# Kernel optimization log

Measured on AMD Instinct MI355X. Metric: run time of the kernel, lower is better.

## Reference

```python
import jax, jax.numpy as jnp
import numpy as np

N = 50000      # nodes
E = 800000     # edges
F_IN = 128     # input features
H = 8          # heads
F = 16         # features per head
NEG_SLOPE = 0.2


def setup_inputs() -> dict:
    key = jax.random.key(0)
    k_x, k_ei, k_w, k_as, k_ad = jax.random.split(key, 5)
    x = jax.random.normal(k_x, (N, F_IN), dtype=jnp.float32)
    edge_index = jax.random.randint(k_ei, (2, E), 0, N, dtype=jnp.int64)
    # learned params (PyG GATConv: lin weight [H*F, F_in] no bias; att_src/att_dst [H, F]; out bias [H*F])
    glorot = lambda k, shp: jax.random.uniform(k, shp, jnp.float32, -1.0, 1.0) * np.sqrt(6.0 / (shp[-1] + shp[-2]))
    W = glorot(k_w, (H * F, F_IN))
    att_src = glorot(k_as, (H, F))
    att_dst = glorot(k_ad, (H, F))
    bias = jnp.zeros((H * F,), dtype=jnp.float32)  # bias_init = zeros_
    return {"x": x, "W": W, "att_src": att_src, "att_dst": att_dst, "bias": bias, "edge_index": edge_index}


def reference(x, W, att_src, att_dst, bias, edge_index):
    # linear projection, split heads: [N, H, F]
    h = (x @ W.T).reshape(N, H, F)
    # per-node attention logits: [N, H]
    a_src = jnp.einsum('nhf,hf->nh', h, att_src)
    a_dst = jnp.einsum('nhf,hf->nh', h, att_dst)
    src, dst = edge_index[0], edge_index[1]
    # edge scores + LeakyReLU: [E, H]
    e = a_src[src] + a_dst[dst]
    e = jnp.where(e >= 0, e, NEG_SLOPE * e)
    # segment softmax over incoming edges of each dst node
    m = jax.ops.segment_max(e, dst, num_segments=N)          # [N, H]
    ex = jnp.exp(e - m[dst])                                  # [E, H]
    denom = jax.ops.segment_sum(ex, dst, num_segments=N)     # [N, H]
    alpha = ex / (denom[dst] + 1e-16)                         # [E, H]
    # weighted scatter-aggregate of source features
    msg = alpha[:, :, None] * h[src]                          # [E, H, F]
    out = jax.ops.segment_sum(msg, dst, num_segments=N)      # [N, H, F]
    return out.reshape(N, H * F) + bias
```

## Files before the change

### kernel.cpp

```cpp
#include <hip/hip_runtime.h>

#define NEG_SLOPE 0.2f
#define HEADS 8
#define FEAT 16
#define HF 128
#define FIN 128
#define BROWS 64
#define PITCH 136
#define BSHIFT 6
#define BNODES 64
#define MAXBUCK 1024
#define EPT 16
#define SCAP 32
#define CAP 2048

typedef __bf16 bf16x8 __attribute__((ext_vector_type(8)));
typedef float  f32x4  __attribute__((ext_vector_type(4)));

__device__ __forceinline__ bool detect_i64(const int* ei) {
    return (ei[1] | ei[3] | ei[5] | ei[7]) == 0;
}
__device__ __forceinline__ int load_idx(const int* ei, long long pos, bool is64) {
    return is64 ? ei[2 * pos] : ei[pos];
}

__device__ __forceinline__ float bf2f(unsigned u) { return __uint_as_float(u << 16); }

__device__ __forceinline__ unsigned short f2bf(float f) {
    unsigned u = __float_as_uint(f);
    unsigned r = u + 0x7fffu + ((u >> 16) & 1u);
    return (unsigned short)(r >> 16);
}

__global__ __launch_bounds__(256) void proj_binsort_kernel(
    const float* __restrict__ x, const float* __restrict__ W,
    const float* __restrict__ att_src, const float* __restrict__ att_dst,
    unsigned short* __restrict__ hb, float* __restrict__ a_src,
    float* __restrict__ a_dst,
    const int* __restrict__ ei, unsigned* __restrict__ ebuf,
    int* __restrict__ cnt2, int N, int E, int nb, int nsb, int PB)
{
    __shared__ __align__(16) char smem[(BROWS + FIN) * PITCH * 2];
    const int t = threadIdx.x;

    if (blockIdx.x >= PB) {
        int* lh = (int*)smem;
        const int blk = blockIdx.x - PB;
        const bool is64 = detect_i64(ei);
        const int e0 = blk * (EPT * 256);

        for (int b = t; b < nb; b += 256) lh[b] = 0;
        __syncthreads();

#pragma unroll
        for (int i = 0; i < EPT; ++i) {
            const int e = e0 + i * 256 + t;
            if (e < E) {
                const unsigned s = (unsigned)load_idx(ei, e, is64);
                const unsigned d = (unsigned)load_idx(ei, (long long)E + e, is64);
                const unsigned pk = s | (d << 16);
                const int bkt = d >> BSHIFT;
                const int ofs = atomicAdd(&lh[bkt], 1);
                if (ofs < SCAP)
                    ebuf[((size_t)bkt * nsb + blk) * SCAP + ofs] = pk;
            }
        }
        __syncthreads();
        for (int b = t; b < nb; b += 256)
            cnt2[blk * MAXBUCK + b] = min(lh[b], SCAP);
        return;
    }

    unsigned short* xs  = (unsigned short*)smem;
    unsigned short* wsl = xs + BROWS * PITCH;
    const int n0 = blockIdx.x * BROWS;

#pragma unroll
    for (int i = 0; i < 8; ++i) {
        const int f4 = i * 256 + t;
        const int r = f4 >> 5, c4 = f4 & 31;
        const int rr = (n0 + r < N) ? (n0 + r) : (N - 1);
        const float4 v = ((const float4*)(x + (size_t)rr * FIN))[c4];
        unsigned short* p = &xs[r * PITCH + c4 * 4];
        p[0] = f2bf(v.x); p[1] = f2bf(v.y); p[2] = f2bf(v.z); p[3] = f2bf(v.w);
    }
#pragma unroll
    for (int i = 0; i < 16; ++i) {
        const int f4 = i * 256 + t;
        const int r = f4 >> 5, c4 = f4 & 31;
        const float4 v = ((const float4*)(W + (size_t)r * FIN))[c4];
        unsigned short* p = &wsl[r * PITCH + c4 * 4];
        p[0] = f2bf(v.x); p[1] = f2bf(v.y); p[2] = f2bf(v.z); p[3] = f2bf(v.w);
    }
    __syncthreads();

    const int w = t >> 6, lane = t & 63;
    const int lrow = lane & 15;
    const int lk = lane >> 4;
    const int r0 = w * 16;

    f32x4 acc[8];
#pragma unroll
    for (int i = 0; i < 8; ++i) { f32x4 z = {0.f, 0.f, 0.f, 0.f}; acc[i] = z; }

#pragma unroll
    for (int ks = 0; ks < 4; ++ks) {
        const int kb = ks * 32 + lk * 8;
        const bf16x8 af = *(const bf16x8*)&xs[(r0 + lrow) * PITCH + kb];
#pragma unroll
        for (int tt = 0; tt < 8; ++tt) {
            const bf16x8 bf = *(const bf16x8*)&wsl[(tt * 16 + lrow) * PITCH + kb];
            acc[tt] = __builtin_amdgcn_mfma_f32_16x16x32_bf16(af, bf, acc[tt], 0, 0, 0);
        }
    }
    __syncthreads();

#pragma unroll
    for (int tt = 0; tt < 8; ++tt) {
#pragma unroll
        for (int rg = 0; rg < 4; ++rg) {
            const int row = r0 + lk * 4 + rg;
            const int col = tt * 16 + lrow;
            xs[row * PITCH + col] = f2bf(acc[tt][rg]);
        }
    }
    __syncthreads();

#pragma unroll
    for (int i = 0; i < 8; ++i) {
        const int u4 = i * 256 + t;
        const int r = u4 >> 5, c4 = u4 & 31;
        if (n0 + r < N) {
            const unsigned short* p = &xs[r * PITCH + c4 * 4];
            ushort4 v; v.x = p[0]; v.y = p[1]; v.z = p[2]; v.w = p[3];
            ((ushort4*)hb)[(size_t)(n0 + r) * (HF / 4) + c4] = v;
        }
    }
#pragma unroll
    for (int i = 0; i < 2; ++i) {
        const int p = i * 256 + t;
        const int r = p >> 3, hd = p & 7;
        if (n0 + r < N) {
            float s = 0.f, d = 0.f;
#pragma unroll
            for (int j = 0; j < FEAT; ++j) {
                const float hv = bf2f(xs[r * PITCH + hd * FEAT + j]);
                s = fmaf(hv, att_src[hd * FEAT + j], s);
                d = fmaf(hv, att_dst[hd * FEAT + j], d);
            }
            a_src[(size_t)(n0 + r) * HEADS + hd] = s;
            a_dst[(size_t)(n0 + r) * HEADS + hd] = d;
        }
    }
}

__global__ __launch_bounds__(256) void bucket_agg(
    const unsigned* __restrict__ ebuf, const int* __restrict__ cnt2,
    const float* __restrict__ a_src, const float* __restrict__ a_dst,
    const unsigned short* __restrict__ hb, const float* __restrict__ bias,
    float* __restrict__ out, int N, int nsb)
{
    __shared__ int soff[256];
    __shared__ unsigned ubuf[CAP];
    __shared__ unsigned srt[CAP];
    __shared__ int cnts[BNODES], sc[BNODES], cur[BNODES];
    const int b = blockIdx.x;
    const int t = threadIdx.x;

    const int v = (t < nsb) ? cnt2[t * MAXBUCK + b] : 0;
    soff[t] = v;
    __syncthreads();
#pragma unroll
    for (int off = 1; off < 256; off <<= 1) {
        const int y = (t >= off) ? soff[t - off] : 0;
        __syncthreads();
        soff[t] += y;
        __syncthreads();
    }
    const int cntb = min(soff[255], CAP);
    const int myoff = soff[t] - v;
    __syncthreads();

    if (t < nsb && v > 0) {
        const unsigned* sp = ebuf + ((size_t)b * nsb + t) * SCAP;
        for (int j = 0; j < v; ++j) {
            const int o = myoff + j;
            if (o < CAP) ubuf[o] = sp[j];
        }
    }
    if (t < BNODES) cnts[t] = 0;
    __syncthreads();

    for (int j = t; j < cntb; j += 256)
        atomicAdd(&cnts[(ubuf[j] >> 16) & (BNODES - 1)], 1);
    __syncthreads();
    if (t < BNODES) sc[t] = cnts[t];
    __syncthreads();
#pragma unroll
    for (int off = 1; off < BNODES; off <<= 1) {
        const int y = (t < BNODES && t >= off) ? sc[t - off] : 0;
        __syncthreads();
        if (t < BNODES) sc[t] += y;
        __syncthreads();
    }
    if (t < BNODES) cur[t] = sc[t] - cnts[t];
    __syncthreads();
    for (int j = t; j < cntb; j += 256) {
        const unsigned p = ubuf[j];
        const int dl = (p >> 16) & (BNODES - 1);
        const int ofs = atomicAdd(&cur[dl], 1);
        srt[ofs] = p & 0xffffu;
    }
    __syncthreads();

    const int w = t >> 6, lane = t & 63;
    const int hd = lane >> 3;
    const float2 b2 = ((const float2*)bias)[lane];

#pragma unroll 1
    for (int i = 0; i < BNODES / 4; ++i) {
        const int dl = w * (BNODES / 4) + i;
        const int d = b * BNODES + dl;
        if (d >= N) break;
        const int end = sc[dl];
        const int beg = end - cnts[dl];
        const float adh = a_dst[d * HEADS + hd];

        float acc0 = 0.f, acc1 = 0.f, den = 0.f;
        int j = beg;
        for (; j + 8 <= end; j += 8) {
            int s[8]; unsigned p[8]; float wg[8];
#pragma unroll
            for (int k = 0; k < 8; ++k) s[k] = (int)srt[j + k];
#pragma unroll
            for (int k = 0; k < 8; ++k)
                p[k] = *(const unsigned*)(hb + (size_t)s[k] * HF + 2 * lane);
#pragma unroll
            for (int k = 0; k < 8; ++k) {
                float vv = a_src[s[k] * HEADS + hd] + adh;
                vv = vv >= 0.f ? vv : NEG_SLOPE * vv;
                wg[k] = __expf(vv);
            }
#pragma unroll
            for (int k = 0; k < 8; ++k) {
                acc0 = fmaf(wg[k], bf2f(p[k] & 0xffffu), acc0);
                acc1 = fmaf(wg[k], bf2f(p[k] >> 16),     acc1);
                den += wg[k];
            }
        }
        for (; j + 4 <= end; j += 4) {
            int s[4]; unsigned p[4]; float wg[4];
#pragma unroll
            for (int k = 0; k < 4; ++k) s[k] = (int)srt[j + k];
#pragma unroll
            for (int k = 0; k < 4; ++k)
                p[k] = *(const unsigned*)(hb + (size_t)s[k] * HF + 2 * lane);
#pragma unroll
            for (int k = 0; k < 4; ++k) {
                float vv = a_src[s[k] * HEADS + hd] + adh;
                vv = vv >= 0.f ? vv : NEG_SLOPE * vv;
                wg[k] = __expf(vv);
            }
#pragma unroll
            for (int k = 0; k < 4; ++k) {
                acc0 = fmaf(wg[k], bf2f(p[k] & 0xffffu), acc0);
                acc1 = fmaf(wg[k], bf2f(p[k] >> 16),     acc1);
                den += wg[k];
            }
        }
        for (; j < end; ++j) {
            const int s = (int)srt[j];
            const unsigned p = *(const unsigned*)(hb + (size_t)s * HF + 2 * lane);
            float vv = a_src[s * HEADS + hd] + adh;
            vv = vv >= 0.f ? vv : NEG_SLOPE * vv;
            const float wg = __expf(vv);
            acc0 = fmaf(wg, bf2f(p & 0xffffu), acc0);
            acc1 = fmaf(wg, bf2f(p >> 16), acc1);
            den += wg;
        }
        const float inv = 1.f / (den + 1e-16f);
        float2 o2;
        o2.x = fmaf(acc0, inv, b2.x);
        o2.y = fmaf(acc1, inv, b2.y);
        ((float2*)out)[(size_t)d * (HF / 2) + lane] = o2;
    }
}

extern "C" void kernel_launch(void* const* d_in, const int* in_sizes, int n_in,
                              void* d_out, int out_size, void* d_ws, size_t ws_size,
                              hipStream_t stream)
{
    const float* x       = (const float*)d_in[0];
    const float* W       = (const float*)d_in[1];
    const float* att_src = (const float*)d_in[2];
    const float* att_dst = (const float*)d_in[3];
    const float* bias    = (const float*)d_in[4];
    const int*   ei      = (const int*)d_in[5];
    float* out = (float*)d_out;

    const int N = in_sizes[0] / FIN;
    const int E = in_sizes[5] / 2;
    const int NBUCK = (N + BNODES - 1) >> BSHIFT;
    const int NSB = (E + EPT * 256 - 1) / (EPT * 256);
    const int PB = (N + BROWS - 1) / BROWS;

    char* ws = (char*)d_ws;
    unsigned short* hb = (unsigned short*)ws; ws += (size_t)N * HF * 2;
    unsigned* ebuf = (unsigned*)ws; ws += (size_t)NBUCK * NSB * SCAP * 4;
    int* cnt2      = (int*)ws;  ws += (size_t)NSB * MAXBUCK * sizeof(int);
    float* a_src  = (float*)ws; ws += (size_t)N * HEADS * sizeof(float);
    float* a_dst  = (float*)ws; ws += (size_t)N * HEADS * sizeof(float);

    hipLaunchKernelGGL(proj_binsort_kernel, dim3(PB + NSB), dim3(256), 0, stream,
                       x, W, att_src, att_dst, hb, a_src, a_dst,
                       ei, ebuf, cnt2, N, E, NBUCK, NSB, PB);
    hipLaunchKernelGGL(bucket_agg, dim3(NBUCK), dim3(256), 0, stream,
                       ebuf, cnt2, a_src, a_dst, hb, bias, out, N, NSB);
}
```

Measured before the change: 161.5 us.

## Halve destination buckets and replace shared-memory scans with wavefront shuffle scans

Bucket size drops from 64 to 32 destination nodes, which doubles the number of aggregation blocks and shrinks the per-bucket staging buffers and shared memory. The two block-level prefix scans, one over per-source-block counts and one over per-node counts, now use wavefront shuffle scans instead of shared-memory scans with a barrier at every step, removing many __syncthreads. The risks are smaller per-segment capacity (SCAP 20, CAP 1024), which could overflow on skewed degree distributions, and each block now does the same setup work for half as many nodes.

```diff
diff --git a/kernel.cpp b/kernel.cpp
--- a/kernel.cpp
+++ b/kernel.cpp
@@ -7,12 +7,12 @@
 #define FIN 128
 #define BROWS 64
 #define PITCH 136
-#define BSHIFT 6
-#define BNODES 64
-#define MAXBUCK 1024
+#define BSHIFT 5
+#define BNODES 32
+#define MAXBUCK 2048
 #define EPT 16
-#define SCAP 32
-#define CAP 2048
+#define SCAP 20
+#define CAP 1024
 
 typedef __bf16 bf16x8 __attribute__((ext_vector_type(8)));
 typedef float  f32x4  __attribute__((ext_vector_type(4)));
@@ -160,26 +160,33 @@
     const unsigned short* __restrict__ hb, const float* __restrict__ bias,
     float* __restrict__ out, int N, int nsb)
 {
-    __shared__ int soff[256];
     __shared__ unsigned ubuf[CAP];
     __shared__ unsigned srt[CAP];
     __shared__ int cnts[BNODES], sc[BNODES], cur[BNODES];
+    __shared__ int wsum[4];
     const int b = blockIdx.x;
     const int t = threadIdx.x;
+    const int w = t >> 6, lane = t & 63;
 
     const int v = (t < nsb) ? cnt2[t * MAXBUCK + b] : 0;
-    soff[t] = v;
-    __syncthreads();
-#pragma unroll
-    for (int off = 1; off < 256; off <<= 1) {
-        const int y = (t >= off) ? soff[t - off] : 0;
-        __syncthreads();
-        soff[t] += y;
-        __syncthreads();
-    }
-    const int cntb = min(soff[255], CAP);
-    const int myoff = soff[t] - v;
-    __syncthreads();
+    int x = v;
+#pragma unroll
+    for (int off = 1; off < 64; off <<= 1) {
+        const int y = __shfl_up(x, off, 64);
+        if (lane >= off) x += y;
+    }
+    if (lane == 63) wsum[w] = x;
+    __syncthreads();
+    int add = 0, tot = 0;
+#pragma unroll
+    for (int i = 0; i < 4; ++i) {
+        const int ws_i = wsum[i];
+        if (i < w) add += ws_i;
+        tot += ws_i;
+    }
+    const int incl = x + add;
+    const int myoff = incl - v;
+    const int cntb = min(tot, CAP);
 
     if (t < nsb && v > 0) {
         const unsigned* sp = ebuf + ((size_t)b * nsb + t) * SCAP;
@@ -194,17 +201,20 @@
     for (int j = t; j < cntb; j += 256)
         atomicAdd(&cnts[(ubuf[j] >> 16) & (BNODES - 1)], 1);
     __syncthreads();
-    if (t < BNODES) sc[t] = cnts[t];
-    __syncthreads();
-#pragma unroll
-    for (int off = 1; off < BNODES; off <<= 1) {
-        const int y = (t < BNODES && t >= off) ? sc[t - off] : 0;
-        __syncthreads();
-        if (t < BNODES) sc[t] += y;
-        __syncthreads();
-    }
-    if (t < BNODES) cur[t] = sc[t] - cnts[t];
-    __syncthreads();
+
+    if (t < BNODES) {
+        const int c = cnts[t];
+        int sx = c;
+#pragma unroll
+        for (int off = 1; off < BNODES; off <<= 1) {
+            const int y = __shfl_up(sx, off, 64);
+            if (t >= off) sx += y;
+        }
+        sc[t] = sx;
+        cur[t] = sx - c;
+    }
+    __syncthreads();
+
     for (int j = t; j < cntb; j += 256) {
         const unsigned p = ubuf[j];
         const int dl = (p >> 16) & (BNODES - 1);
@@ -213,7 +223,6 @@
     }
     __syncthreads();
 
-    const int w = t >> 6, lane = t & 63;
     const int hd = lane >> 3;
     const float2 b2 = ((const float2*)bias)[lane];
 
```

Result: faster. 157.6 us (-2.4%).
